# Kernel tuning notes

Hardware: AMD Instinct MI355X
Metric: run time of the kernel (lower is better)

The kernel has to match this reference:

```python
import jax, jax.numpy as jnp
import numpy as np

EPS = 1e-5
B, S, E = 4, 2048, 2048
H, DH = 16, 128
F = 8192


def rmsnorm(x, gamma):
    # Keras LayerNormalization(rms_scaling=True): x * rsqrt(mean(x^2)+eps) * gamma
    return x * jax.lax.rsqrt(jnp.mean(jnp.square(x), axis=-1, keepdims=True) + EPS) * gamma


def rope(x, positions, head_dim):
    # Rotary embedding applied per head_dim-sized chunk of the embedding axis
    b, s, e = x.shape
    x = x.reshape(b, s, e // head_dim, head_dim)
    half = head_dim // 2
    inv_freq = 1.0 / (10000.0 ** (jnp.arange(half, dtype=x.dtype) / half))  # [half]
    ang = positions.astype(x.dtype)[:, None] * inv_freq  # [S, half]
    cos = jnp.concatenate([jnp.cos(ang), jnp.cos(ang)], axis=-1)[None, :, None, :]
    sin = jnp.concatenate([jnp.sin(ang), jnp.sin(ang)], axis=-1)[None, :, None, :]
    x1, x2 = x[..., :half], x[..., half:]
    rot = jnp.concatenate([-x2, x1], axis=-1)
    return (x * cos + rot * sin).reshape(b, s, e)


def setup_inputs() -> dict:
    key = jax.random.key(0)
    ks = jax.random.split(key, 12)
    std = 0.02
    return {
        "inputs": jax.random.normal(ks[0], (B, S, E), dtype=jnp.float32),
        "gamma_attn": jnp.ones((E,), dtype=jnp.float32),
        "gamma_ffn": jnp.ones((E,), dtype=jnp.float32),
        "wq": jax.random.normal(ks[1], (E, H, DH), dtype=jnp.float32) * std,
        "wk": jax.random.normal(ks[2], (E, H, DH), dtype=jnp.float32) * std,
        "wv": jax.random.normal(ks[3], (E, H, DH), dtype=jnp.float32) * std,
        "wo": jax.random.normal(ks[4], (H, DH, E), dtype=jnp.float32) * std,
        "w_gate": jax.random.normal(ks[5], (E, F), dtype=jnp.float32) * std,
        "w_lin": jax.random.normal(ks[6], (E, F), dtype=jnp.float32) * std,
        "w_out": jax.random.normal(ks[7], (F, E), dtype=jnp.float32) * std,
        "positions": jnp.arange(S, dtype=jnp.int32),
        "cache": jnp.zeros((1,), dtype=jnp.int32),
        "mask": jnp.ones((B, S), dtype=bool),
    }


def reference(inputs, gamma_attn, gamma_ffn, wq, wk, wv, wo, w_gate, w_lin, w_out, positions, cache, mask):
    x = inputs
    # --- attention sub-block ---
    y = rmsnorm(x, gamma_attn)
    y = rope(y, positions, DH)
    q = jnp.einsum("bse,ehd->bshd", y, wq)
    k = jnp.einsum("bse,ehd->bshd", y, wk)
    v = jnp.einsum("bse,ehd->bshd", y, wv)
    scores = jnp.einsum("bqhd,bkhd->bhqk", q, k) / jnp.sqrt(jnp.asarray(DH, q.dtype))
    causal = jnp.tril(jnp.ones((S, S), dtype=bool))
    scores = jnp.where(causal[None, None], scores, jnp.asarray(-1e9, scores.dtype))
    probs = jax.nn.softmax(scores, axis=-1)
    attn = jnp.einsum("bhqk,bkhd->bqhd", probs, v)
    y = jnp.einsum("bqhd,hde->bqe", attn, wo)
    x = y + x
    # --- FFN sub-block (gelu-gated) ---
    y = rmsnorm(x, gamma_ffn)
    y = jnp.einsum("bse,ef->bsf", jax.nn.gelu(y @ w_gate, approximate=False) * (y @ w_lin), jnp.eye(F, dtype=y.dtype)) if False else (jax.nn.gelu(y @ w_gate, approximate=False) * (y @ w_lin)) @ w_out
    return y + x
```

## Files before the change

kernel.cpp:

```cpp
#include <hip/hip_runtime.h>
#include <cstdint>
#include <cstddef>

#define B_ 4
#define S_ 2048
#define E_ 2048
#define H_ 16
#define DH_ 128
#define F_ 8192
#define NTOK (B_*S_)
#define QKVN (3*E_)

typedef __attribute__((ext_vector_type(4))) float f32x4;
typedef __attribute__((ext_vector_type(8))) __bf16 bf16x8;
typedef __attribute__((ext_vector_type(8))) short s16x8;
typedef __attribute__((ext_vector_type(4))) short s16x4;

using gas_ptr = const __attribute__((address_space(1))) void*;
using las_ptr = __attribute__((address_space(3))) void*;

__device__ __forceinline__ short f2bf(float f) {
  union { float f; uint32_t u; } v{f};
  uint32_t r = v.u + 0x7FFFu + ((v.u >> 16) & 1u);
  return (short)(r >> 16);
}
__device__ __forceinline__ float bf2f(short s) {
  union { uint32_t u; float f; } v;
  v.u = ((uint32_t)(uint16_t)s) << 16;
  return v.f;
}

__global__ __launch_bounds__(256) void k_rms_rope(const float* __restrict__ x,
                                                  const float* __restrict__ gamma,
                                                  const int* __restrict__ pos,
                                                  short* __restrict__ y) {
  const int row = blockIdx.x;
  const int s = row & (S_ - 1);
  const int t = threadIdx.x;
  const int head = t >> 4;
  const int j0 = (t & 15) << 2;
  const float* xr = x + (size_t)row * E_;
  const int c1 = head * DH_ + j0;
  const int c2 = c1 + 64;
  f32x4 x1 = *(const f32x4*)(xr + c1);
  f32x4 x2 = *(const f32x4*)(xr + c2);
  float ss = x1[0]*x1[0]+x1[1]*x1[1]+x1[2]*x1[2]+x1[3]*x1[3]
           + x2[0]*x2[0]+x2[1]*x2[1]+x2[2]*x2[2]+x2[3]*x2[3];
  #pragma unroll
  for (int off = 32; off >= 1; off >>= 1) ss += __shfl_xor(ss, off, 64);
  __shared__ float red[4];
  __shared__ float rsh;
  if ((t & 63) == 0) red[t >> 6] = ss;
  __syncthreads();
  if (t == 0) rsh = rsqrtf((red[0]+red[1]+red[2]+red[3]) * (1.0f / E_) + 1e-5f);
  __syncthreads();
  const float r = rsh;
  f32x4 g1 = *(const f32x4*)(gamma + c1);
  f32x4 g2 = *(const f32x4*)(gamma + c2);
  const float p = (float)pos[s];
  s16x4 o1, o2;
  #pragma unroll
  for (int jj = 0; jj < 4; ++jj) {
    float fi = exp2f((float)(j0 + jj) * (-13.287712379549449f / 64.0f));
    float ang = p * fi;
    float sn, cs;
    sincosf(ang, &sn, &cs);
    float a = x1[jj] * r * g1[jj];
    float b = x2[jj] * r * g2[jj];
    o1[jj] = f2bf(a * cs - b * sn);
    o2[jj] = f2bf(b * cs + a * sn);
  }
  *(s16x4*)(y + (size_t)row * E_ + c1) = o1;
  *(s16x4*)(y + (size_t)row * E_ + c2) = o2;
}

__global__ __launch_bounds__(256) void k_rms(const float* __restrict__ x,
                                             const float* __restrict__ gamma,
                                             short* __restrict__ y) {
  const int row = blockIdx.x;
  const int t = threadIdx.x;
  const int c = t << 3;
  const float* xr = x + (size_t)row * E_;
  f32x4 a = *(const f32x4*)(xr + c);
  f32x4 b = *(const f32x4*)(xr + c + 4);
  float ss = a[0]*a[0]+a[1]*a[1]+a[2]*a[2]+a[3]*a[3]
           + b[0]*b[0]+b[1]*b[1]+b[2]*b[2]+b[3]*b[3];
  #pragma unroll
  for (int off = 32; off >= 1; off >>= 1) ss += __shfl_xor(ss, off, 64);
  __shared__ float red[4];
  __shared__ float rsh;
  if ((t & 63) == 0) red[t >> 6] = ss;
  __syncthreads();
  if (t == 0) rsh = rsqrtf((red[0]+red[1]+red[2]+red[3]) * (1.0f / E_) + 1e-5f);
  __syncthreads();
  const float r = rsh;
  f32x4 ga = *(const f32x4*)(gamma + c);
  f32x4 gb = *(const f32x4*)(gamma + c + 4);
  s16x8 o;
  #pragma unroll
  for (int jj = 0; jj < 4; ++jj) {
    o[jj]   = f2bf(a[jj] * r * ga[jj]);
    o[4+jj] = f2bf(b[jj] * r * gb[jj]);
  }
  *(s16x8*)(y + (size_t)row * E_ + c) = o;
}

__global__ __launch_bounds__(256) void k_transpose_f32_bf16(const float* __restrict__ src,
                                                            short* __restrict__ dst,
                                                            int R, int C) {
  __shared__ float tile[32][33];
  const int c0 = blockIdx.x << 5, r0 = blockIdx.y << 5;
  const int tx = threadIdx.x & 31, ty = threadIdx.x >> 5;
  #pragma unroll
  for (int j = 0; j < 32; j += 8)
    tile[ty + j][tx] = src[(size_t)(r0 + ty + j) * C + c0 + tx];
  __syncthreads();
  #pragma unroll
  for (int j = 0; j < 32; j += 8)
    dst[(size_t)(c0 + ty + j) * R + r0 + tx] = f2bf(tile[tx][ty + j]);
}

__global__ __launch_bounds__(256) void k_transpose_v(const short* __restrict__ qkv,
                                                     short* __restrict__ vt) {
  __shared__ short tile[32][33];
  const int bh = blockIdx.z;
  const short* src = qkv + (size_t)(bh >> 4) * S_ * QKVN + 2 * E_ + (bh & 15) * DH_;
  short* dst = vt + (size_t)bh * DH_ * S_;
  const int s0 = blockIdx.x << 5, d0 = blockIdx.y << 5;
  const int tx = threadIdx.x & 31, ty = threadIdx.x >> 5;
  #pragma unroll
  for (int j = 0; j < 32; j += 8)
    tile[ty + j][tx] = src[(size_t)(s0 + ty + j) * QKVN + d0 + tx];
  __syncthreads();
  #pragma unroll
  for (int j = 0; j < 32; j += 8)
    dst[(size_t)(d0 + ty + j) * S_ + s0 + tx] = tile[tx][ty + j];
}

template<int EPI>
__global__ __launch_bounds__(256, 3) void k_gemm(const short* __restrict__ A,
                                                 const short* __restrict__ Bt,
                                                 void* Cv, const void* aux,
                                                 int M, int N, int K) {
  __shared__ short As[128 * 64];
  __shared__ short Bs[128 * 64];
  const int tiles_n = gridDim.x, tiles_m = gridDim.y;
  const int bid = blockIdx.y * tiles_n + blockIdx.x;
  const int GM = 16;
  const int band = bid / (GM * tiles_n);
  const int first_m = band * GM;
  const int bandh = min(GM, tiles_m - first_m);
  const int rem = bid - band * GM * tiles_n;
  const int m_tile = first_m + rem % bandh;
  const int n_tile = rem / bandh;
  const int n0 = n_tile << 7, m0 = m_tile << 7;

  const int tid = threadIdx.x;
  const int wave = tid >> 6, lane = tid & 63;
  const int ll = lane & 15, lh = lane >> 4;
  const int wm = wave >> 1, wn = wave & 1;
  const int lr = lane >> 3, lc = lane & 7;
  const int lcs = lc ^ lr;
  const short* Ag = A  + (size_t)(m0 + wave * 32 + lr) * K + lcs * 8;
  const short* Bg = Bt + (size_t)(n0 + wave * 32 + lr) * K + lcs * 8;
  const int sw = ll & 7;
  const f32x4 fzero = {0.f, 0.f, 0.f, 0.f};
  f32x4 acc[4][4];
  #pragma unroll
  for (int i = 0; i < 4; ++i)
    #pragma unroll
    for (int j = 0; j < 4; ++j) acc[i][j] = fzero;

  for (int k0 = 0; k0 < K; k0 += 64) {
    __syncthreads();
    #pragma unroll
    for (int i = 0; i < 4; ++i) {
      __builtin_amdgcn_global_load_lds((gas_ptr)(Ag + (size_t)(i * 8) * K),
                                       (las_ptr)&As[(wave * 32 + i * 8) * 64], 16, 0, 0);
      __builtin_amdgcn_global_load_lds((gas_ptr)(Bg + (size_t)(i * 8) * K),
                                       (las_ptr)&Bs[(wave * 32 + i * 8) * 64], 16, 0, 0);
    }
    Ag += 64; Bg += 64;
    __syncthreads();
    #pragma unroll
    for (int kc = 0; kc < 2; ++kc) {
      bf16x8 af[4], bfr[4];
      const int pcg = ((kc * 4 + lh) ^ sw) * 8;
      #pragma unroll
      for (int mt = 0; mt < 4; ++mt)
        af[mt] = *(const bf16x8*)&As[(wm * 64 + mt * 16 + ll) * 64 + pcg];
      #pragma unroll
      for (int nt = 0; nt < 4; ++nt)
        bfr[nt] = *(const bf16x8*)&Bs[(wn * 64 + nt * 16 + ll) * 64 + pcg];
      #pragma unroll
      for (int mt = 0; mt < 4; ++mt)
        #pragma unroll
        for (int nt = 0; nt < 4; ++nt)
          acc[mt][nt] = __builtin_amdgcn_mfma_f32_16x16x32_bf16(af[mt], bfr[nt], acc[mt][nt], 0, 0, 0);
    }
  }
  #pragma unroll
  for (int mt = 0; mt < 4; ++mt) {
    const int row = m0 + wm * 64 + mt * 16 + lh * 4;
    #pragma unroll
    for (int nt = 0; nt < 4; ++nt) {
      const int col = n0 + wn * 64 + nt * 16 + ll;
      #pragma unroll
      for (int rg = 0; rg < 4; ++rg) {
        const float c = acc[mt][nt][rg];
        const size_t idx = (size_t)(row + rg) * N + col;
        if constexpr (EPI == 0) {
          ((short*)Cv)[idx] = f2bf(c);
        } else if constexpr (EPI == 1) {
          ((float*)Cv)[idx] = c + ((const float*)aux)[idx];
        } else if constexpr (EPI == 2) {
          float g = 0.5f * c * (1.0f + erff(c * 0.70710678118654752f));
          ((short*)Cv)[idx] = f2bf(g);
        } else {
          float g = bf2f(((short*)Cv)[idx]);
          ((short*)Cv)[idx] = f2bf(c * g);
        }
      }
    }
  }
}

#define CEXP 0.12752682475470602f
__global__ __launch_bounds__(256, 2) void k_flash(const short* __restrict__ qkv,
                                                  const short* __restrict__ vt,
                                                  short* __restrict__ attn) {
  __shared__ short Kt[64][136];
  __shared__ short VtT[128][72];
  __shared__ short Pt[4][32][72];
  const int qt = blockIdx.x, bh = blockIdx.y;
  const int b = bh >> 4, h = bh & 15;
  const int q0 = qt << 7;
  const int tid = threadIdx.x, wave = tid >> 6, lane = tid & 63;
  const int ll = lane & 15, lh = lane >> 4;
  const short* qbase = qkv + (size_t)b * S_ * QKVN + h * DH_;
  const short* kbase = qbase + E_;
  const short* vbase = vt + (size_t)bh * DH_ * S_;

  bf16x8 qf[2][4];
  #pragma unroll
  for (int mt = 0; mt < 2; ++mt) {
    const short* qr = qbase + (size_t)(q0 + wave * 32 + mt * 16 + ll) * QKVN;
    #pragma unroll
    for (int kc = 0; kc < 4; ++kc) qf[mt][kc] = *(const bf16x8*)(qr + kc * 32 + lh * 8);
  }

  const f32x4 fzero = {0.f, 0.f, 0.f, 0.f};
  float m_i[2][4], l_i[2][4];
  f32x4 oacc[2][8];
  #pragma unroll
  for (int mt = 0; mt < 2; ++mt) {
    #pragma unroll
    for (int rg = 0; rg < 4; ++rg) { m_i[mt][rg] = -1e30f; l_i[mt][rg] = 0.f; }
    #pragma unroll
    for (int n8 = 0; n8 < 8; ++n8) oacc[mt][n8] = fzero;
  }

  const int nkt = (q0 + 128) >> 6;
  for (int kt = 0; kt < nkt; ++kt) {
    const int k0 = kt << 6;
    __syncthreads();
    #pragma unroll
    for (int p = 0; p < 4; ++p) {
      int idx = p * 256 + tid;
      int r = idx >> 4, c0 = (idx & 15) << 3;
      *(s16x8*)&Kt[r][c0] = *(const s16x8*)(kbase + (size_t)(k0 + r) * QKVN + c0);
      int dh = idx >> 3, kk = (idx & 7) << 3;
      *(s16x8*)&VtT[dh][kk] = *(const s16x8*)(vbase + (size_t)dh * S_ + k0 + kk);
    }
    __syncthreads();

    f32x4 sc[2][4];
    #pragma unroll
    for (int mt = 0; mt < 2; ++mt)
      #pragma unroll
      for (int nt = 0; nt < 4; ++nt) sc[mt][nt] = fzero;
    #pragma unroll
    for (int kc = 0; kc < 4; ++kc) {
      bf16x8 kb[4];
      #pragma unroll
      for (int nt = 0; nt < 4; ++nt)
        kb[nt] = *(const bf16x8*)&Kt[nt * 16 + ll][kc * 32 + lh * 8];
      #pragma unroll
      for (int mt = 0; mt < 2; ++mt)
        #pragma unroll
        for (int nt = 0; nt < 4; ++nt)
          sc[mt][nt] = __builtin_amdgcn_mfma_f32_16x16x32_bf16(qf[mt][kc], kb[nt], sc[mt][nt], 0, 0, 0);
    }

    if (k0 + 63 > q0) {
      #pragma unroll
      for (int mt = 0; mt < 2; ++mt)
        #pragma unroll
        for (int nt = 0; nt < 4; ++nt)
          #pragma unroll
          for (int rg = 0; rg < 4; ++rg) {
            int kidx = k0 + nt * 16 + ll;
            int qidx = q0 + wave * 32 + mt * 16 + lh * 4 + rg;
            if (kidx > qidx) sc[mt][nt][rg] = -1e30f;
          }
    }

    #pragma unroll
    for (int mt = 0; mt < 2; ++mt)
      #pragma unroll
      for (int rg = 0; rg < 4; ++rg) {
        float mx = fmaxf(fmaxf(sc[mt][0][rg], sc[mt][1][rg]),
                         fmaxf(sc[mt][2][rg], sc[mt][3][rg]));
        #pragma unroll
        for (int off = 1; off < 16; off <<= 1) mx = fmaxf(mx, __shfl_xor(mx, off, 64));
        float mn = fmaxf(m_i[mt][rg], mx);
        float al = exp2f((m_i[mt][rg] - mn) * CEXP);
        m_i[mt][rg] = mn;
        float rsum = 0.f;
        #pragma unroll
        for (int nt = 0; nt < 4; ++nt) {
          float pv = exp2f((sc[mt][nt][rg] - mn) * CEXP);
          sc[mt][nt][rg] = pv;
          rsum += pv;
        }
        #pragma unroll
        for (int off = 1; off < 16; off <<= 1) rsum += __shfl_xor(rsum, off, 64);
        l_i[mt][rg] = l_i[mt][rg] * al + rsum;
        #pragma unroll
        for (int n8 = 0; n8 < 8; ++n8) oacc[mt][n8][rg] *= al;
      }

    #pragma unroll
    for (int mt = 0; mt < 2; ++mt)
      #pragma unroll
      for (int nt = 0; nt < 4; ++nt)
        #pragma unroll
        for (int rg = 0; rg < 4; ++rg)
          Pt[wave][mt * 16 + lh * 4 + rg][nt * 16 + ll] = f2bf(sc[mt][nt][rg]);

    #pragma unroll
    for (int kc2 = 0; kc2 < 2; ++kc2) {
      bf16x8 pa[2];
      #pragma unroll
      for (int mt = 0; mt < 2; ++mt)
        pa[mt] = *(const bf16x8*)&Pt[wave][mt * 16 + ll][kc2 * 32 + lh * 8];
      #pragma unroll
      for (int n8 = 0; n8 < 8; ++n8) {
        bf16x8 vb = *(const bf16x8*)&VtT[n8 * 16 + ll][kc2 * 32 + lh * 8];
        #pragma unroll
        for (int mt = 0; mt < 2; ++mt)
          oacc[mt][n8] = __builtin_amdgcn_mfma_f32_16x16x32_bf16(pa[mt], vb, oacc[mt][n8], 0, 0, 0);
      }
    }
  }

  short* ab = attn + (size_t)(b * S_) * E_ + h * DH_;
  #pragma unroll
  for (int mt = 0; mt < 2; ++mt) {
    const int row = q0 + wave * 32 + mt * 16 + lh * 4;
    #pragma unroll
    for (int n8 = 0; n8 < 8; ++n8) {
      const int col = n8 * 16 + ll;
      #pragma unroll
      for (int rg = 0; rg < 4; ++rg)
        ab[(size_t)(row + rg) * E_ + col] = f2bf(oacc[mt][n8][rg] / l_i[mt][rg]);
    }
  }
}

extern "C" void kernel_launch(void* const* d_in, const int* in_sizes, int n_in,
                              void* d_out, int out_size, void* d_ws, size_t ws_size,
                              hipStream_t stream) {
  (void)in_sizes; (void)n_in; (void)out_size; (void)ws_size;
  const float* x      = (const float*)d_in[0];
  const float* g_attn = (const float*)d_in[1];
  const float* g_ffn  = (const float*)d_in[2];
  const float* wq     = (const float*)d_in[3];
  const float* wk     = (const float*)d_in[4];
  const float* wv     = (const float*)d_in[5];
  const float* wo     = (const float*)d_in[6];
  const float* wg     = (const float*)d_in[7];
  const float* wl     = (const float*)d_in[8];
  const float* wout   = (const float*)d_in[9];
  const int*   pos    = (const int*)d_in[10];

  char* wsb = (char*)d_ws;
  short* W    = (short*)wsb;
  short* BIG  = (short*)(wsb + (size_t)33554432);
  short* ACT  = (short*)(wsb + (size_t)33554432 + 134217728);

  short* QKV  = BIG;
  short* VT   = BIG + (size_t)NTOK * QKVN;
  short* Hb   = BIG;
  short* Y1   = ACT;
  short* ATTN = ACT;
  short* Y2   = ACT;
  float* X2   = (float*)d_out;

  const dim3 blk(256);

  k_transpose_f32_bf16<<<dim3(64, 64), blk, 0, stream>>>(wq, W,                   2048, 2048);
  k_transpose_f32_bf16<<<dim3(64, 64), blk, 0, stream>>>(wk, W + 2048 * 2048,     2048, 2048);
  k_transpose_f32_bf16<<<dim3(64, 64), blk, 0, stream>>>(wv, W + 2 * 2048 * 2048, 2048, 2048);

  k_rms_rope<<<NTOK, blk, 0, stream>>>(x, g_attn, pos, Y1);
  k_gemm<0><<<dim3(QKVN / 128, NTOK / 128), blk, 0, stream>>>(Y1, W, QKV, nullptr, NTOK, QKVN, E_);
  k_transpose_v<<<dim3(S_ / 32, DH_ / 32, B_ * H_), blk, 0, stream>>>(QKV, VT);
  k_flash<<<dim3(S_ / 128, B_ * H_), blk, 0, stream>>>(QKV, VT, ATTN);

  k_transpose_f32_bf16<<<dim3(64, 64), blk, 0, stream>>>(wo, W, 2048, 2048);
  k_gemm<1><<<dim3(E_ / 128, NTOK / 128), blk, 0, stream>>>(ATTN, W, X2, x, NTOK, E_, E_);

  k_rms<<<NTOK, blk, 0, stream>>>(X2, g_ffn, Y2);

  k_transpose_f32_bf16<<<dim3(256, 64), blk, 0, stream>>>(wg, W, 2048, 8192);
  k_gemm<2><<<dim3(F_ / 128, NTOK / 128), blk, 0, stream>>>(Y2, W, Hb, nullptr, NTOK, F_, E_);
  k_transpose_f32_bf16<<<dim3(256, 64), blk, 0, stream>>>(wl, W, 2048, 8192);
  k_gemm<3><<<dim3(F_ / 128, NTOK / 128), blk, 0, stream>>>(Y2, W, Hb, nullptr, NTOK, F_, E_);
  k_transpose_f32_bf16<<<dim3(64, 256), blk, 0, stream>>>(wout, W, 8192, 2048);
  k_gemm<1><<<dim3(E_ / 128, NTOK / 128), blk, 0, stream>>>(Hb, W, d_out, X2, NTOK, E_, F_);
}
```

Before: 1.823 ms.

## Rewrite GEMM as 256x256-tile, 512-thread, multi-stage pipelined kernel

Replaces the 128x128 single-buffered GEMM with a 256x256 tile computed by 8 waves. It uses a 5-slot A and 4-slot B LDS ring filled by direct global-to-LDS loads issued several half-steps ahead, so loads overlap the MFMA work. It also adds s_setprio around the MFMA bursts, an XOR swizzle for LDS reads, and an XCD-aware remapping of block IDs. The aim is to hide global latency and raise data reuse per block, at the cost of more registers, more LDS, fewer blocks in flight, and intricate hand-written waitcnt and barrier sequencing that could be fragile.

Measured after the change: 2.112 ms. +15.9%, slower.

```diff
diff --git a/kernel.cpp b/kernel.cpp
--- a/kernel.cpp
+++ b/kernel.cpp
@@ -138,87 +138,160 @@
 }
 
 template<int EPI>
-__global__ __launch_bounds__(256, 3) void k_gemm(const short* __restrict__ A,
+__global__ __launch_bounds__(512, 2) void k_gemm(const short* __restrict__ A,
                                                  const short* __restrict__ Bt,
                                                  void* Cv, const void* aux,
                                                  int M, int N, int K) {
-  __shared__ short As[128 * 64];
-  __shared__ short Bs[128 * 64];
-  const int tiles_n = gridDim.x, tiles_m = gridDim.y;
-  const int bid = blockIdx.y * tiles_n + blockIdx.x;
-  const int GM = 16;
-  const int band = bid / (GM * tiles_n);
-  const int first_m = band * GM;
-  const int bandh = min(GM, tiles_m - first_m);
-  const int rem = bid - band * GM * tiles_n;
-  const int m_tile = first_m + rem % bandh;
-  const int n_tile = rem / bandh;
-  const int n0 = n_tile << 7, m0 = m_tile << 7;
+  __shared__ __align__(16) short As[5 * 256 * 32];
+  __shared__ __align__(16) short Bs[4 * 256 * 32];
+  const int tiles_n = gridDim.x;
+  const int nwg = tiles_n * (int)gridDim.y;
+  int bid = (int)blockIdx.y * tiles_n + (int)blockIdx.x;
+  if ((nwg & 7) == 0) bid = (bid & 7) * (nwg >> 3) + (bid >> 3);
+  const int m_tile = bid / tiles_n, n_tile = bid - m_tile * tiles_n;
+  const int m0 = m_tile << 8, n0 = n_tile << 8;
 
   const int tid = threadIdx.x;
   const int wave = tid >> 6, lane = tid & 63;
   const int ll = lane & 15, lh = lane >> 4;
-  const int wm = wave >> 1, wn = wave & 1;
-  const int lr = lane >> 3, lc = lane & 7;
-  const int lcs = lc ^ lr;
-  const short* Ag = A  + (size_t)(m0 + wave * 32 + lr) * K + lcs * 8;
-  const short* Bg = Bt + (size_t)(n0 + wave * 32 + lr) * K + lcs * 8;
-  const int sw = ll & 7;
-  const f32x4 fzero = {0.f, 0.f, 0.f, 0.f};
-  f32x4 acc[4][4];
-  #pragma unroll
-  for (int i = 0; i < 4; ++i)
-    #pragma unroll
-    for (int j = 0; j < 4; ++j) acc[i][j] = fzero;
-
-  for (int k0 = 0; k0 < K; k0 += 64) {
-    __syncthreads();
-    #pragma unroll
-    for (int i = 0; i < 4; ++i) {
-      __builtin_amdgcn_global_load_lds((gas_ptr)(Ag + (size_t)(i * 8) * K),
-                                       (las_ptr)&As[(wave * 32 + i * 8) * 64], 16, 0, 0);
-      __builtin_amdgcn_global_load_lds((gas_ptr)(Bg + (size_t)(i * 8) * K),
-                                       (las_ptr)&Bs[(wave * 32 + i * 8) * 64], 16, 0, 0);
-    }
-    Ag += 64; Bg += 64;
-    __syncthreads();
-    #pragma unroll
-    for (int kc = 0; kc < 2; ++kc) {
-      bf16x8 af[4], bfr[4];
-      const int pcg = ((kc * 4 + lh) ^ sw) * 8;
-      #pragma unroll
-      for (int mt = 0; mt < 4; ++mt)
-        af[mt] = *(const bf16x8*)&As[(wm * 64 + mt * 16 + ll) * 64 + pcg];
-      #pragma unroll
-      for (int nt = 0; nt < 4; ++nt)
-        bfr[nt] = *(const bf16x8*)&Bs[(wn * 64 + nt * 16 + ll) * 64 + pcg];
-      #pragma unroll
-      for (int mt = 0; mt < 4; ++mt)
-        #pragma unroll
-        for (int nt = 0; nt < 4; ++nt)
-          acc[mt][nt] = __builtin_amdgcn_mfma_f32_16x16x32_bf16(af[mt], bfr[nt], acc[mt][nt], 0, 0, 0);
-    }
-  }
-  #pragma unroll
-  for (int mt = 0; mt < 4; ++mt) {
-    const int row = m0 + wm * 64 + mt * 16 + lh * 4;
-    #pragma unroll
-    for (int nt = 0; nt < 4; ++nt) {
-      const int col = n0 + wn * 64 + nt * 16 + ll;
+  const int wm = wave >> 2, wn = wave & 3;
+
+  const int sr0 = tid >> 2;
+  const int g = (tid & 3) ^ ((sr0 & 3) ^ ((sr0 >> 2) & 3));
+  const short* Ag0 = A  + (size_t)(m0 + sr0) * K + g * 8;
+  const short* Bg0 = Bt + (size_t)(n0 + sr0) * K + g * 8;
+  const size_t rstep = (size_t)128 * K;
+  const int wuB = wave << 9;
+
+  const int NKT = K >> 6;
+  const int HMAX = NKT << 2;
+
+  auto STAGE = [&](int h) {
+    if (h > HMAX - 1) h = HMAX - 1;
+    const int sidx = h >> 1;
+    const int koff = ((h >> 2) << 6) + (((h >> 1) & 1) << 5);
+    if ((h & 1) == 0) {
+      const int sl = (sidx % 5) << 13;
+      __builtin_amdgcn_global_load_lds((gas_ptr)(Ag0 + koff),
+                                       (las_ptr)(As + sl + wuB), 16, 0, 0);
+      __builtin_amdgcn_global_load_lds((gas_ptr)(Ag0 + koff + rstep),
+                                       (las_ptr)(As + sl + 4096 + wuB), 16, 0, 0);
+    } else {
+      const int sl = (sidx & 3) << 13;
+      __builtin_amdgcn_global_load_lds((gas_ptr)(Bg0 + koff),
+                                       (las_ptr)(Bs + sl + wuB), 16, 0, 0);
+      __builtin_amdgcn_global_load_lds((gas_ptr)(Bg0 + koff + rstep),
+                                       (las_ptr)(Bs + sl + 4096 + wuB), 16, 0, 0);
+    }
+  };
+
+  const f32x4 fz = {0.f, 0.f, 0.f, 0.f};
+  f32x4 acc[8][4];
+  #pragma unroll
+  for (int i = 0; i < 8; ++i)
+    #pragma unroll
+    for (int j = 0; j < 4; ++j) acc[i][j] = fz;
+
+  const int sA = (ll & 3) ^ ((ll >> 2) & 3);
+  const int cOff = (lh ^ sA) << 3;
+  const int rdA = (((wm << 7) + ll) << 5) + cOff;
+  const int rdB = (((wn << 6) + ll) << 5) + cOff;
+
+  #pragma unroll
+  for (int h = 0; h < 7; ++h) STAGE(h);
+  asm volatile("s_waitcnt vmcnt(6)" ::: "memory");
+  __builtin_amdgcn_s_barrier();
+
+  for (int kt = 0; kt < NKT; ++kt) {
+    const int hb = (kt << 2) + 7;
+    const int slA0 = ((2 * kt) % 5) << 13;
+    const int slA1 = ((2 * kt + 1) % 5) << 13;
+    const int slB0 = ((2 * kt) & 3) << 13;
+    const int slB1 = slB0 + (1 << 13);
+    bf16x8 bA[4], bB[4];
+
+    #pragma unroll
+    for (int nf = 0; nf < 4; ++nf) bB[nf] = *(const bf16x8*)&Bs[slB0 + rdB + nf * 512];
+    #pragma unroll
+    for (int mf = 0; mf < 4; ++mf) bA[mf] = *(const bf16x8*)&As[slA0 + rdA + mf * 512];
+    STAGE(hb);
+    __builtin_amdgcn_s_barrier();
+    asm volatile("s_waitcnt lgkmcnt(0)" ::: "memory");
+    __builtin_amdgcn_s_setprio(1);
+    #pragma unroll
+    for (int mf = 0; mf < 4; ++mf)
+      #pragma unroll
+      for (int nf = 0; nf < 4; ++nf)
+        acc[mf][nf] = __builtin_amdgcn_mfma_f32_16x16x32_bf16(bA[mf], bB[nf], acc[mf][nf], 0, 0, 0);
+    __builtin_amdgcn_s_setprio(0);
+    __builtin_amdgcn_s_barrier();
+
+    #pragma unroll
+    for (int mf = 0; mf < 4; ++mf) bA[mf] = *(const bf16x8*)&As[slA0 + rdA + 2048 + mf * 512];
+    STAGE(hb + 1);
+    __builtin_amdgcn_s_barrier();
+    asm volatile("s_waitcnt lgkmcnt(0)" ::: "memory");
+    __builtin_amdgcn_s_setprio(1);
+    #pragma unroll
+    for (int mf = 0; mf < 4; ++mf)
+      #pragma unroll
+      for (int nf = 0; nf < 4; ++nf)
+        acc[4 + mf][nf] = __builtin_amdgcn_mfma_f32_16x16x32_bf16(bA[mf], bB[nf], acc[4 + mf][nf], 0, 0, 0);
+    __builtin_amdgcn_s_setprio(0);
+    __builtin_amdgcn_s_barrier();
+
+    #pragma unroll
+    for (int nf = 0; nf < 4; ++nf) bB[nf] = *(const bf16x8*)&Bs[slB1 + rdB + nf * 512];
+    #pragma unroll
+    for (int mf = 0; mf < 4; ++mf) bA[mf] = *(const bf16x8*)&As[slA1 + rdA + mf * 512];
+    STAGE(hb + 2);
+    __builtin_amdgcn_s_barrier();
+    asm volatile("s_waitcnt lgkmcnt(0)" ::: "memory");
+    __builtin_amdgcn_s_setprio(1);
+    #pragma unroll
+    for (int mf = 0; mf < 4; ++mf)
+      #pragma unroll
+      for (int nf = 0; nf < 4; ++nf)
+        acc[mf][nf] = __builtin_amdgcn_mfma_f32_16x16x32_bf16(bA[mf], bB[nf], acc[mf][nf], 0, 0, 0);
+    __builtin_amdgcn_s_setprio(0);
+    __builtin_amdgcn_s_barrier();
+
+    #pragma unroll
+    for (int mf = 0; mf < 4; ++mf) bA[mf] = *(const bf16x8*)&As[slA1 + rdA + 2048 + mf * 512];
+    STAGE(hb + 3);
+    __builtin_amdgcn_s_barrier();
+    asm volatile("s_waitcnt lgkmcnt(0)" ::: "memory");
+    __builtin_amdgcn_s_setprio(1);
+    #pragma unroll
+    for (int mf = 0; mf < 4; ++mf)
+      #pragma unroll
+      for (int nf = 0; nf < 4; ++nf)
+        acc[4 + mf][nf] = __builtin_amdgcn_mfma_f32_16x16x32_bf16(bA[mf], bB[nf], acc[4 + mf][nf], 0, 0, 0);
+    __builtin_amdgcn_s_setprio(0);
+    asm volatile("s_waitcnt vmcnt(6)" ::: "memory");
+    __builtin_amdgcn_s_barrier();
+  }
+
+  #pragma unroll
+  for (int mf = 0; mf < 8; ++mf) {
+    const int row = m0 + (wm << 7) + (mf << 4) + (lh << 2);
+    #pragma unroll
+    for (int nf = 0; nf < 4; ++nf) {
+      const int col = n0 + (wn << 6) + (nf << 4) + ll;
       #pragma unroll
       for (int rg = 0; rg < 4; ++rg) {
-        const float c = acc[mt][nt][rg];
+        const float c = acc[mf][nf][rg];
         const size_t idx = (size_t)(row + rg) * N + col;
         if constexpr (EPI == 0) {
           ((short*)Cv)[idx] = f2bf(c);
         } else if constexpr (EPI == 1) {
           ((float*)Cv)[idx] = c + ((const float*)aux)[idx];
         } else if constexpr (EPI == 2) {
-          float g = 0.5f * c * (1.0f + erff(c * 0.70710678118654752f));
-          ((short*)Cv)[idx] = f2bf(g);
+          float gl = 0.5f * c * (1.0f + erff(c * 0.70710678118654752f));
+          ((short*)Cv)[idx] = f2bf(gl);
         } else {
-          float g = bf2f(((short*)Cv)[idx]);
-          ((short*)Cv)[idx] = f2bf(c * g);
+          float gl = bf2f(((short*)Cv)[idx]);
+          ((short*)Cv)[idx] = f2bf(c * gl);
         }
       }
     }
@@ -398,25 +471,26 @@
   float* X2   = (float*)d_out;
 
   const dim3 blk(256);
+  const dim3 gblk(512);
 
   k_transpose_f32_bf16<<<dim3(64, 64), blk, 0, stream>>>(wq, W,                   2048, 2048);
   k_transpose_f32_bf16<<<dim3(64, 64), blk, 0, stream>>>(wk, W + 2048 * 2048,     2048, 2048);
   k_transpose_f32_bf16<<<dim3(64, 64), blk, 0, stream>>>(wv, W + 2 * 2048 * 2048, 2048, 2048);
 
   k_rms_rope<<<NTOK, blk, 0, stream>>>(x, g_attn, pos, Y1);
-  k_gemm<0><<<dim3(QKVN / 128, NTOK / 128), blk, 0, stream>>>(Y1, W, QKV, nullptr, NTOK, QKVN, E_);
+  k_gemm<0><<<dim3(QKVN / 256, NTOK / 256), gblk, 0, stream>>>(Y1, W, QKV, nullptr, NTOK, QKVN, E_);
   k_transpose_v<<<dim3(S_ / 32, DH_ / 32, B_ * H_), blk, 0, stream>>>(QKV, VT);
   k_flash<<<dim3(S_ / 128, B_ * H_), blk, 0, stream>>>(QKV, VT, ATTN);
 
   k_transpose_f32_bf16<<<dim3(64, 64), blk, 0, stream>>>(wo, W, 2048, 2048);
-  k_gemm<1><<<dim3(E_ / 128, NTOK / 128), blk, 0, stream>>>(ATTN, W, X2, x, NTOK, E_, E_);
+  k_gemm<1><<<dim3(E_ / 256, NTOK / 256), gblk, 0, stream>>>(ATTN, W, X2, x, NTOK, E_, E_);
 
   k_rms<<<NTOK, blk, 0, stream>>>(X2, g_ffn, Y2);
 
   k_transpose_f32_bf16<<<dim3(256, 64), blk, 0, stream>>>(wg, W, 2048, 8192);
-  k_gemm<2><<<dim3(F_ / 128, NTOK / 128), blk, 0, stream>>>(Y2, W, Hb, nullptr, NTOK, F_, E_);
+  k_gemm<2><<<dim3(F_ / 256, NTOK / 256), gblk, 0, stream>>>(Y2, W, Hb, nullptr, NTOK, F_, E_);
   k_transpose_f32_bf16<<<dim3(256, 64), blk, 0, stream>>>(wl, W, 2048, 8192);
-  k_gemm<3><<<dim3(F_ / 128, NTOK / 128), blk, 0, stream>>>(Y2, W, Hb, nullptr, NTOK, F_, E_);
+  k_gemm<3><<<dim3(F_ / 256, NTOK / 256), gblk, 0, stream>>>(Y2, W, Hb, nullptr, NTOK, F_, E_);
   k_transpose_f32_bf16<<<dim3(64, 256), blk, 0, stream>>>(wout, W, 8192, 2048);
-  k_gemm<1><<<dim3(E_ / 128, NTOK / 128), blk, 0, stream>>>(Hb, W, d_out, X2, NTOK, E_, F_);
-}
+  k_gemm<1><<<dim3(E_ / 256, NTOK / 256), gblk, 0, stream>>>(Hb, W, d_out, X2, NTOK, E_, F_);
+}
```
